# Performance work log

Measured on AMD Instinct MI355X. Metric: run time of the kernel, lower is better.

Reference implementation:

```python
import jax, jax.numpy as jnp
import numpy as np

B, C, L, H, W = 8, 768, 8, 14, 14
HEADS = 12
HD = C // HEADS
SCALE = HD ** (-0.5)
KQ, SQ, PQ = (3, 3, 3), (1, 1, 1), (1, 1, 1)
KKV, SKV, PKV = (3, 3, 3), (1, 2, 2), (1, 1, 1)
EPS = 1e-6


def setup_inputs() -> dict:
    key = jax.random.key(0)
    ks = jax.random.split(key, 16)
    s = 0.02
    inp = {
        'x': jax.random.normal(ks[0], (B, C, L, H, W), jnp.float32),
        'class_token': jax.random.normal(ks[1], (B, C), jnp.float32),
        'Wq': jax.random.normal(ks[2], (C, C), jnp.float32) * s,
        'bq': jnp.zeros((C,), jnp.float32),
        'Wk': jax.random.normal(ks[3], (C, C), jnp.float32) * s,
        'bk': jnp.zeros((C,), jnp.float32),
        'Wv': jax.random.normal(ks[4], (C, C), jnp.float32) * s,
        'bv': jnp.zeros((C,), jnp.float32),
        # depthwise Conv3d kernels: (C, 1, kD, kH, kW), groups=C, no bias
        'conv_q': jax.random.normal(ks[5], (C, 1) + KQ, jnp.float32) * 0.1,
        'conv_k': jax.random.normal(ks[6], (C, 1) + KKV, jnp.float32) * 0.1,
        'conv_v': jax.random.normal(ks[7], (C, 1) + KKV, jnp.float32) * 0.1,
        'lnq_w': jnp.ones((C,), jnp.float32), 'lnq_b': jnp.zeros((C,), jnp.float32),
        'lnk_w': jnp.ones((C,), jnp.float32), 'lnk_b': jnp.zeros((C,), jnp.float32),
        'lnv_w': jnp.ones((C,), jnp.float32), 'lnv_b': jnp.zeros((C,), jnp.float32),
        'Wproj': jax.random.normal(ks[8], (C, C), jnp.float32) * s,
        'bproj': jnp.zeros((C,), jnp.float32),
    }
    return inp


def _linear_keep(x, cls, Wm, b):
    # x: (B,C,l,h,w) -> tokens (B,N,C), prepend cls, linear, split
    Bb, Cc, l, h, w = x.shape
    t = x.reshape(Bb, Cc, -1).transpose(0, 2, 1)          # (B,N,C)
    t = jnp.concatenate([cls[:, None, :], t], axis=1)      # (B,1+N,C)
    y = t @ Wm.T + b
    cls_o = y[:, 0]
    y = y[:, 1:].transpose(0, 2, 1).reshape(Bb, -1, l, h, w)
    return y, cls_o


def _pool(x, wconv, stride, pad, ln_w, ln_b):
    # depthwise 3D conv (groups=C), then LayerNorm over channels
    y = jax.lax.conv_general_dilated(
        x, wconv, window_strides=stride,
        padding=[(p, p) for p in pad],
        dimension_numbers=('NCDHW', 'OIDHW', 'NCDHW'),
        feature_group_count=C)
    y = jnp.moveaxis(y, 1, -1)                            # (B,l,h,w,C)
    mu = y.mean(-1, keepdims=True)
    var = y.var(-1, keepdims=True)
    y = (y - mu) * jax.lax.rsqrt(var + EPS) * ln_w + ln_b
    return jnp.moveaxis(y, -1, 1)


def _to_heads(t):
    # (B,C,l,h,w) -> (B,heads,N,head_dim)
    Bb = t.shape[0]
    return t.reshape(Bb, HEADS, HD, -1).transpose(0, 1, 3, 2)


def _attention(q, k, v, cq, ck, cv, Wp, bp, out_lhw):
    Bb = q.shape[0]
    q = jnp.concatenate([cq.reshape(Bb, HEADS, 1, HD), _to_heads(q)], axis=2)
    k = jnp.concatenate([ck.reshape(Bb, HEADS, 1, HD), _to_heads(k)], axis=2)
    v = jnp.concatenate([cv.reshape(Bb, HEADS, 1, HD), _to_heads(v)], axis=2)
    scores = jnp.einsum('bhqc,bhkc->bhqk', q, k) * SCALE
    attn = jax.nn.softmax(scores, axis=-1)
    o = jnp.einsum('bhqk,bhkc->bhqc', attn, v)            # (B,heads,1+Nq,hd)
    o = o.transpose(0, 2, 1, 3).reshape(Bb, -1, C)        # (B,1+Nq,C)
    o = o @ Wp.T + bp
    cls_o = o[:, 0]
    xo = o[:, 1:].transpose(0, 2, 1).reshape(Bb, C, *out_lhw)
    return xo, cls_o


def reference(x, class_token, Wq, bq, Wk, bk, Wv, bv,
              conv_q, conv_k, conv_v,
              lnq_w, lnq_b, lnk_w, lnk_b, lnv_w, lnv_b,
              Wproj, bproj):
    # pool_first=False: QKV linears first (with cls token), then pooling of the
    # spatial tensors only (cls tokens bypass pooling).
    q, cls_q = _linear_keep(x, class_token, Wq, bq)
    k, cls_k = _linear_keep(x, class_token, Wk, bk)
    v, cls_v = _linear_keep(x, class_token, Wv, bv)
    q = _pool(q, conv_q, SQ, PQ, lnq_w, lnq_b)
    k = _pool(k, conv_k, SKV, PKV, lnk_w, lnk_b)
    v = _pool(v, conv_v, SKV, PKV, lnv_w, lnv_b)
    out_lhw = q.shape[2:]
    return _attention(q, k, v, cls_q, cls_k, cls_v, Wproj, bproj, out_lhw)
```

## Files before the change

### kernel.cpp

```cpp
#include <hip/hip_runtime.h>

#define CDIM 768
#define BATCH 8
#define LDEPTH 8
#define HHEIGHT 14
#define WWIDTH 14
#define NSP 1568
#define NSPX 1576
#define NQTOK 1569
#define NKSP 392
#define NKTOK 393
#define NHEADS 12
#define HEADDIM 64
#define ATTN_SCALE 0.125f
#define LN_EPS 1e-6f
#define MTOK (BATCH * NQTOK)
#define NPAD_X 1792
#define WELEM (CDIM * CDIM)
#define TQP 1792
#define TKP 448

typedef _Float16 f16;
typedef _Float16 f16x8_t __attribute__((ext_vector_type(8)));
typedef _Float16 f16x4_t __attribute__((ext_vector_type(4)));
typedef float f32x4_t __attribute__((ext_vector_type(4)));
typedef float f32x2_t __attribute__((ext_vector_type(2)));

__device__ __forceinline__ void gld_lds16(const void* g, void* l) {
  __builtin_amdgcn_global_load_lds(
      (const __attribute__((address_space(1))) void*)g,
      (__attribute__((address_space(3))) void*)l, 16, 0, 0);
}

__global__ __launch_bounds__(256) void convert4_kernel(
    const float* __restrict__ s0, const float* __restrict__ s1,
    const float* __restrict__ s2, const float* __restrict__ s3,
    f16* __restrict__ dst) {
  const int mat = blockIdx.y;
  const float* src = (mat == 0) ? s0 : (mat == 1) ? s1 : (mat == 2) ? s2 : s3;
  int i = (blockIdx.x * 256 + threadIdx.x) * 4;
  if (i < WELEM) {
    float4 v = *(const float4*)&src[i];
    f16x4_t h = {(f16)v.x, (f16)v.y, (f16)v.z, (f16)v.w};
    *(f16x4_t*)&dst[(size_t)mat * WELEM + i] = h;
  }
}

__global__ __launch_bounds__(256) void transpose_x_kernel(
    const float* __restrict__ X, const float* __restrict__ cls,
    f16* __restrict__ Xt) {
  __shared__ float t[32][33];
  const int b = blockIdx.z;
  const int k0 = blockIdx.y * 32;
  const int n0 = blockIdx.x * 32;
  const int tx = threadIdx.x & 31, ty = threadIdx.x >> 5;
#pragma unroll
  for (int i = 0; i < 4; i++) {
    int k = k0 + ty + i * 8;
    int n = n0 + tx;
    float v;
    if (n < NSP)
      v = X[((size_t)b * CDIM + k) * NSP + n];
    else if (n == NSP)
      v = cls[b * CDIM + k];
    else
      v = 0.f;
    t[ty + i * 8][tx] = v;
  }
  __syncthreads();
#pragma unroll
  for (int i = 0; i < 4; i++) {
    int n = n0 + ty + i * 8;
    Xt[((size_t)b * NPAD_X + n) * CDIM + k0 + tx] = (f16)t[tx][ty + i * 8];
  }
}

__global__ __launch_bounds__(256, 2) void gemm_qkv_f16_kernel(
    const f16* __restrict__ W16, const f16* __restrict__ Xt,
    const float* __restrict__ bq, const float* __restrict__ bk,
    const float* __restrict__ bv, f16* __restrict__ OutBase) {
  __shared__ __align__(16) f16 Asm[128 * 32];
  __shared__ __align__(16) f16 Bsm[256 * 32];

  const int bid = blockIdx.x;
  const int b = bid & 7;
  const int rem = bid >> 3;
  const int mat = rem / 42;
  const int rem2 = rem % 42;
  const int m0 = (rem2 / 7) * 128;
  const int n0 = (rem2 % 7) * 256;
  const int tid = threadIdx.x;
  const int lane = tid & 63;
  const int w = tid >> 6;
  const int wr = w >> 1, wc = w & 1;
  const int l15 = lane & 15, l4 = lane >> 4;

  const f16* A16 = W16 + (size_t)mat * WELEM;
  const float* bias = (mat == 0) ? bq : (mat == 1) ? bk : bv;
  f16* Out = OutBase + (size_t)mat * ((size_t)BATCH * CDIM * NSPX);

  const int srow = lane >> 2;
  const int skq = ((lane & 3) ^ ((lane >> 3) & 3)) * 8;
  const f16* Ag = A16 + (size_t)(m0 + w * 32 + srow) * CDIM + skq;
  const f16* Bg = Xt + ((size_t)b * NPAD_X + n0 + w * 64 + srow) * CDIM + skq;
  f16* lA = Asm + w * 32 * 32;
  f16* lB = Bsm + w * 64 * 32;

  const int rsw = (l15 >> 1) & 3;
  const int kchunk = (l4 ^ rsw) * 8;

  f32x4_t acc[4][8];
#pragma unroll
  for (int i = 0; i < 4; i++)
#pragma unroll
    for (int j = 0; j < 8; j++) acc[i][j] = (f32x4_t){0.f, 0.f, 0.f, 0.f};

  for (int k0 = 0; k0 < CDIM; k0 += 32) {
    gld_lds16(Ag + k0, lA);
    gld_lds16(Ag + 16 * CDIM + k0, lA + 16 * 32);
    gld_lds16(Bg + k0, lB);
    gld_lds16(Bg + 16 * CDIM + k0, lB + 16 * 32);
    gld_lds16(Bg + 32 * CDIM + k0, lB + 32 * 32);
    gld_lds16(Bg + 48 * CDIM + k0, lB + 48 * 32);
    __syncthreads();
    f16x8_t af[4];
#pragma unroll
    for (int mi = 0; mi < 4; mi++)
      af[mi] = *(const f16x8_t*)(Asm + (wr * 64 + mi * 16 + l15) * 32 + kchunk);
#pragma unroll
    for (int ni = 0; ni < 8; ni++) {
      f16x8_t bfv =
          *(const f16x8_t*)(Bsm + (wc * 128 + ni * 16 + l15) * 32 + kchunk);
#pragma unroll
      for (int mi = 0; mi < 4; mi++)
        acc[mi][ni] = __builtin_amdgcn_mfma_f32_16x16x32_f16(
            af[mi], bfv, acc[mi][ni], 0, 0, 0);
    }
    __syncthreads();
  }

#pragma unroll
  for (int mi = 0; mi < 4; mi++) {
    const int mbase = m0 + wr * 64 + mi * 16 + l4 * 4;
#pragma unroll
    for (int ni = 0; ni < 8; ni++) {
      const int n = n0 + wc * 128 + ni * 16 + l15;
      if (n < NQTOK) {
#pragma unroll
        for (int r = 0; r < 4; r++) {
          Out[((size_t)b * CDIM + mbase + r) * NSPX + n] =
              (f16)(acc[mi][ni][r] + bias[mbase + r]);
        }
      }
    }
  }
}

__global__ __launch_bounds__(256, 2) void gemm_proj_f16_kernel(
    const f16* __restrict__ Wp16, const f16* __restrict__ o16,
    const float* __restrict__ bias, float* __restrict__ xo,
    float* __restrict__ cls_o) {
  __shared__ __align__(16) f16 Asm[128 * 32];
  __shared__ __align__(16) f16 Bsm[256 * 32];

  const int bid = blockIdx.x;
  const int xcd = bid & 7, pos_ = bid >> 3;
  const int base = (xcd < 4) ? xcd * 38 : 152 + (xcd - 4) * 37;
  const int wgid = base + pos_;
  const int m0 = (wgid / 50) * 128;
  const int n0 = (wgid % 50) * 256;
  const int tid = threadIdx.x;
  const int lane = tid & 63;
  const int w = tid >> 6;
  const int wr = w >> 1, wc = w & 1;
  const int l15 = lane & 15, l4 = lane >> 4;

  const int srow = lane >> 2;
  const int skq = ((lane & 3) ^ ((lane >> 3) & 3)) * 8;
  const f16* Ag = Wp16 + (size_t)(m0 + srow) * CDIM + skq;
  const f16* Bg = o16 + (size_t)(n0 + w * 64 + srow) * CDIM + skq;
  f16* lA = Asm + w * 32 * 32;
  f16* lB = Bsm + w * 64 * 32;
  const f16* Agw = Ag + (size_t)(w * 32) * CDIM;

  const int rsw = (l15 >> 1) & 3;
  const int kchunk = (l4 ^ rsw) * 8;

  f32x4_t acc[4][8];
#pragma unroll
  for (int i = 0; i < 4; i++)
#pragma unroll
    for (int j = 0; j < 8; j++) acc[i][j] = (f32x4_t){0.f, 0.f, 0.f, 0.f};

  for (int k0 = 0; k0 < CDIM; k0 += 32) {
    gld_lds16(Agw + k0, lA);
    gld_lds16(Agw + 16 * CDIM + k0, lA + 16 * 32);
    gld_lds16(Bg + k0, lB);
    gld_lds16(Bg + 16 * CDIM + k0, lB + 16 * 32);
    gld_lds16(Bg + 32 * CDIM + k0, lB + 32 * 32);
    gld_lds16(Bg + 48 * CDIM + k0, lB + 48 * 32);
    __syncthreads();
    f16x8_t af[4];
#pragma unroll
    for (int mi = 0; mi < 4; mi++)
      af[mi] = *(const f16x8_t*)(Asm + (wr * 64 + mi * 16 + l15) * 32 + kchunk);
#pragma unroll
    for (int ni = 0; ni < 8; ni++) {
      f16x8_t bfv =
          *(const f16x8_t*)(Bsm + (wc * 128 + ni * 16 + l15) * 32 + kchunk);
#pragma unroll
      for (int mi = 0; mi < 4; mi++)
        acc[mi][ni] = __builtin_amdgcn_mfma_f32_16x16x32_f16(
            af[mi], bfv, acc[mi][ni], 0, 0, 0);
    }
    __syncthreads();
  }

#pragma unroll
  for (int ni = 0; ni < 8; ni++) {
    const int tok = n0 + wc * 128 + ni * 16 + l15;
    if (tok < MTOK) {
      const int bb = tok / NQTOK;
      const int nn = tok % NQTOK;
#pragma unroll
      for (int mi = 0; mi < 4; mi++) {
        const int mbase = m0 + wr * 64 + mi * 16 + l4 * 4;
#pragma unroll
        for (int r = 0; r < 4; r++) {
          float v = acc[mi][ni][r] + bias[mbase + r];
          if (nn == 0)
            cls_o[bb * CDIM + mbase + r] = v;
          else
            xo[((size_t)bb * CDIM + mbase + r) * (size_t)NSP + nn - 1] = v;
        }
      }
    }
  }
}

__global__ __launch_bounds__(256) void dwconv_q_kernel(
    const f16* __restrict__ q_lin, const float* __restrict__ cq,
    f16* __restrict__ q_pool) {
  __shared__ float vol[16 * 196];
  __shared__ float wsm[27];
  const int c = blockIdx.x % CDIM;
  const int b = blockIdx.x / CDIM;
  const f16* xb = q_lin + ((size_t)b * CDIM + c) * (size_t)NSPX;

  for (int i = threadIdx.x; i < 16 * 196; i += 256) vol[i] = 0.f;
  if (threadIdx.x < 27) wsm[threadIdx.x] = cq[c * 27 + threadIdx.x];
  __syncthreads();
  for (int i = threadIdx.x; i < NSP; i += 256) {
    int li = i / 196;
    int r = i - li * 196;
    int hi = r / 14;
    int wi = r - hi * 14;
    vol[(wi + 1) * 196 + (hi + 1) * 12 + (li + 1)] = (float)xb[i];
  }
  __syncthreads();

  if (threadIdx.x < 196) {
    const int ho = threadIdx.x / 14;
    const int wo = threadIdx.x - ho * 14;
    float sums[8];
#pragma unroll
    for (int lo = 0; lo < 8; lo++) sums[lo] = 0.f;
#pragma unroll
    for (int kh = 0; kh < 3; kh++) {
#pragma unroll
      for (int kw = 0; kw < 3; kw++) {
        const float* p = &vol[(wo + kw) * 196 + (ho + kh) * 12];
        float z[10];
        *(f32x4_t*)&z[0] = *(const f32x4_t*)p;
        *(f32x4_t*)&z[4] = *(const f32x4_t*)(p + 4);
        *(f32x2_t*)&z[8] = *(const f32x2_t*)(p + 8);
        const float w0 = wsm[0 + kh * 3 + kw];
        const float w1 = wsm[9 + kh * 3 + kw];
        const float w2 = wsm[18 + kh * 3 + kw];
#pragma unroll
        for (int lo = 0; lo < 8; lo++) {
          sums[lo] = fmaf(z[lo], w0, sums[lo]);
          sums[lo] = fmaf(z[lo + 1], w1, sums[lo]);
          sums[lo] = fmaf(z[lo + 2], w2, sums[lo]);
        }
      }
    }
    f16* ob = q_pool + ((size_t)b * CDIM + c) * (size_t)NSP;
    const int hw = ho * 14 + wo;
#pragma unroll
    for (int lo = 0; lo < 8; lo++) ob[lo * 196 + hw] = (f16)sums[lo];
  }
}

__global__ __launch_bounds__(256) void dwconv_kv_kernel(
    const f16* __restrict__ k_lin, const f16* __restrict__ v_lin,
    const float* __restrict__ ck, const float* __restrict__ cv,
    f16* __restrict__ k_pool, f16* __restrict__ v_pool) {
  __shared__ float vol4[4][16 * 196];
  __shared__ float wsm4[4][27];
  const int which = blockIdx.y;
  const f16* X = which ? v_lin : k_lin;
  const float* wconv = which ? cv : ck;
  f16* Out = which ? v_pool : k_pool;
  const int cg = blockIdx.x % (CDIM / 4);
  const int b = blockIdx.x / (CDIM / 4);
  const int c0 = cg * 4;
  const f16* xb0 = X + ((size_t)b * CDIM + c0) * (size_t)NSPX;

  for (int i = threadIdx.x; i < 4 * 16 * 196; i += 256)
    ((float*)vol4)[i] = 0.f;
  if (threadIdx.x < 108) {
    int ch = threadIdx.x / 27;
    int j = threadIdx.x - ch * 27;
    wsm4[ch][j] = wconv[(c0 + ch) * 27 + j];
  }
  __syncthreads();
  for (int i = threadIdx.x; i < 4 * NSP; i += 256) {
    int ch = i / NSP;
    int j = i - ch * NSP;
    int li = j / 196;
    int r = j - li * 196;
    int hi = r / 14;
    int wi = r - hi * 14;
    vol4[ch][(wi + 1) * 196 + (hi + 1) * 12 + (li + 1)] =
        (float)xb0[(size_t)ch * NSPX + j];
  }
  __syncthreads();

  if (threadIdx.x < 196) {
    const int ch = threadIdx.x / 49;
    const int p2 = threadIdx.x - ch * 49;
    const int ho = p2 / 7;
    const int wo = p2 - ho * 7;
    const float* vol = vol4[ch];
    const float* wsm = wsm4[ch];
    float sums[8];
#pragma unroll
    for (int lo = 0; lo < 8; lo++) sums[lo] = 0.f;
#pragma unroll
    for (int kh = 0; kh < 3; kh++) {
#pragma unroll
      for (int kw = 0; kw < 3; kw++) {
        const float* p = &vol[(wo * 2 + kw) * 196 + (ho * 2 + kh) * 12];
        float z[10];
        *(f32x4_t*)&z[0] = *(const f32x4_t*)p;
        *(f32x4_t*)&z[4] = *(const f32x4_t*)(p + 4);
        *(f32x2_t*)&z[8] = *(const f32x2_t*)(p + 8);
        const float w0 = wsm[0 + kh * 3 + kw];
        const float w1 = wsm[9 + kh * 3 + kw];
        const float w2 = wsm[18 + kh * 3 + kw];
#pragma unroll
        for (int lo = 0; lo < 8; lo++) {
          sums[lo] = fmaf(z[lo], w0, sums[lo]);
          sums[lo] = fmaf(z[lo + 1], w1, sums[lo]);
          sums[lo] = fmaf(z[lo + 2], w2, sums[lo]);
        }
      }
    }
    f16* ob = Out + ((size_t)b * CDIM + c0 + ch) * (size_t)NKSP;
    const int hw = ho * 7 + wo;
#pragma unroll
    for (int lo = 0; lo < 8; lo++) ob[lo * 49 + hw] = (f16)sums[lo];
  }
}

__global__ __launch_bounds__(256) void ln_pack_qk2_kernel(
    const f16* __restrict__ qp, const f16* __restrict__ kp,
    const float* __restrict__ lnq_w, const float* __restrict__ lnq_b,
    const float* __restrict__ lnk_w, const float* __restrict__ lnk_b,
    f16* __restrict__ Qh, f16* __restrict__ Kh) {
  const int bx = blockIdx.x;
  const bool isq = bx < 49;
  const f16* xp = isq ? qp : kp;
  const float* ln_w = isq ? lnq_w : lnk_w;
  const float* ln_b = isq ? lnq_b : lnk_b;
  f16* OutH = isq ? Qh : Kh;
  const int np = isq ? NSP : NKSP;
  const int tp = isq ? TQP : TKP;
  const int b = blockIdx.y;
  const int p0 = (isq ? bx : bx - 49) * 32;
  const int tid = threadIdx.x;
  const int pl = tid & 31;
  const int grp = tid >> 5;
  const int pos = p0 + pl;
  const bool act = pos < np;
  const f16* Xb = xp + (size_t)b * CDIM * (size_t)np;

  __shared__ __align__(16) f16 tile[32][784];
  __shared__ float r1[8][33], r2[8][33];
  __shared__ float smean[32], srstd[32];

  const int swz = (pl & 7) << 3;
  float s1 = 0.f, s2 = 0.f;
  for (int cc = 0; cc < 12; cc++) {
    const int c0 = grp * 96 + cc * 8;
    f16x8_t hv;
#pragma unroll
    for (int i = 0; i < 8; i++) {
      f16 h = act ? Xb[(size_t)(c0 + i) * np + pos] : (f16)0.f;
      hv[i] = h;
      float v = (float)h;
      s1 += v;
      s2 = fmaf(v, v, s2);
    }
    *(f16x8_t*)&tile[pl][c0 ^ swz] = hv;
  }
  r1[grp][pl] = s1;
  r2[grp][pl] = s2;
  __syncthreads();
  if (tid < 32) {
    float t1 = 0.f, t2 = 0.f;
#pragma unroll
    for (int g = 0; g < 8; g++) { t1 += r1[g][tid]; t2 += r2[g][tid]; }
    float mean = t1 * (1.f / 768.f);
    float var = t2 * (1.f / 768.f) - mean * mean;
    smean[tid] = mean;
    srstd[tid] = rsqrtf(var + LN_EPS);
  }
  __syncthreads();

  const int tl = tid >> 3, d8 = (tid & 7) * 8;
  const float mean = smean[tl], rstd = srstd[tl];
  const bool wv = (p0 + tl) < np;
  const int tswz = (tl & 7) << 3;
#pragma unroll
  for (int h = 0; h < NHEADS; h++) {
    const int c = h * 64 + d8;
    f16x8_t raw = *(const f16x8_t*)&tile[tl][c ^ tswz];
    float4 w1 = *(const float4*)&ln_w[c];
    float4 w2 = *(const float4*)&ln_w[c + 4];
    float4 b1 = *(const float4*)&ln_b[c];
    float4 b2 = *(const float4*)&ln_b[c + 4];
    f16x8_t ov;
    ov[0] = (f16)(((float)raw[0] - mean) * rstd * w1.x + b1.x);
    ov[1] = (f16)(((float)raw[1] - mean) * rstd * w1.y + b1.y);
    ov[2] = (f16)(((float)raw[2] - mean) * rstd * w1.z + b1.z);
    ov[3] = (f16)(((float)raw[3] - mean) * rstd * w1.w + b1.w);
    ov[4] = (f16)(((float)raw[4] - mean) * rstd * w2.x + b2.x);
    ov[5] = (f16)(((float)raw[5] - mean) * rstd * w2.y + b2.y);
    ov[6] = (f16)(((float)raw[6] - mean) * rstd * w2.z + b2.z);
    ov[7] = (f16)(((float)raw[7] - mean) * rstd * w2.w + b2.w);
    if (wv)
      *(uint4*)(OutH +
                (((size_t)(b * NHEADS + h)) * (size_t)tp + (p0 + tl + 1)) * 64 +
                d8) = *(uint4*)&ov;
  }
}

__global__ __launch_bounds__(256) void ln_pack_v_kernel(
    const f16* __restrict__ vp, const f16* __restrict__ vlin,
    const float* __restrict__ ln_w, const float* __restrict__ ln_b,
    f16* __restrict__ Vht) {
  const int b = blockIdx.y;
  const int t0 = blockIdx.x * 32;
  const int tid = threadIdx.x;
  const int pl = tid & 31;
  const int grp = tid >> 5;
  const int t = t0 + pl;
  const int pos = t - 1;
  const bool isv = (t >= 1) && (t < NKTOK);
  const f16* Vb = vp + (size_t)b * CDIM * (size_t)NKSP;

  __shared__ float r1[8][33], r2[8][33];
  __shared__ float smean[32], srstd[32];
  __shared__ __align__(16) f16 vtile[128][40];

  float s1 = 0.f, s2 = 0.f;
  if (isv) {
    for (int c = grp; c < CDIM; c += 8) {
      float v = (float)Vb[(size_t)c * NKSP + pos];
      s1 += v;
      s2 = fmaf(v, v, s2);
    }
  }
  r1[grp][pl] = s1;
  r2[grp][pl] = s2;
  __syncthreads();
  if (tid < 32) {
    float t1 = 0.f, t2 = 0.f;
#pragma unroll
    for (int g = 0; g < 8; g++) { t1 += r1[g][tid]; t2 += r2[g][tid]; }
    float mean = t1 * (1.f / 768.f);
    float var = t2 * (1.f / 768.f) - mean * mean;
    smean[tid] = mean;
    srstd[tid] = rsqrtf(var + LN_EPS);
  }
  __syncthreads();
  const float mean = smean[pl], rstd = srstd[pl];

  for (int cc = 0; cc < 6; cc++) {
#pragma unroll
    for (int i = 0; i < 16; i++) {
      int cl = grp * 16 + i;
      int c = cc * 128 + cl;
      float outv;
      if (isv)
        outv = ((float)Vb[(size_t)c * NKSP + pos] - mean) * rstd * ln_w[c] +
               ln_b[c];
      else if (t == 0)
        outv = (float)vlin[((size_t)b * CDIM + c) * NSPX + NSP];
      else
        outv = 0.f;
      vtile[cl][pl] = (f16)outv;
    }
    __syncthreads();
#pragma unroll
    for (int it = 0; it < 2; it++) {
      int idx = it * 256 + tid;
      int cl = idx >> 2, t8 = (idx & 3) * 8;
      uint4 vv = *(const uint4*)&vtile[cl][t8];
      *(uint4*)(Vht + ((size_t)b * CDIM + cc * 128 + cl) * (size_t)TKP + t0 +
                t8) = vv;
    }
    __syncthreads();
  }
}

__global__ __launch_bounds__(768) void cls_fill_kernel(
    const f16* __restrict__ qlin, const f16* __restrict__ klin,
    f16* __restrict__ Qh, f16* __restrict__ Kh) {
  const int b = blockIdx.x;
  const int c = threadIdx.x;
  Qh[(((size_t)(b * NHEADS + (c >> 6))) * TQP) * 64 + (c & 63)] =
      qlin[((size_t)b * CDIM + c) * NSPX + NSP];
  Kh[(((size_t)(b * NHEADS + (c >> 6))) * TKP) * 64 + (c & 63)] =
      klin[((size_t)b * CDIM + c) * NSPX + NSP];
}

__global__ __launch_bounds__(256) void attn_mfma_kernel(
    const f16* __restrict__ Qh, const f16* __restrict__ Kh,
    const f16* __restrict__ Vht, f16* __restrict__ o16) {
  __shared__ __align__(16) f16 Ks[64 * 72];
  __shared__ __align__(16) f16 Vt[64 * 72];
  const int qt = blockIdx.x, h = blockIdx.y, b = blockIdx.z;
  const int tid = threadIdx.x;
  const int lane = tid & 63;
  const int w = tid >> 6;
  const int l15 = lane & 15, l4 = lane >> 4;
  const int q0 = qt * 256 + w * 64;

  const f16* Qp = Qh + ((size_t)(b * NHEADS + h) * TQP) * 64;
  const f16* Kp = Kh + ((size_t)(b * NHEADS + h) * TKP) * 64;
  const f16* Vp = Vht + ((size_t)(b * NHEADS + h) * 64) * TKP;

  f16x8_t bq[4][2];
#pragma unroll
  for (int qi = 0; qi < 4; qi++)
#pragma unroll
    for (int kf = 0; kf < 2; kf++)
      bq[qi][kf] = *(const f16x8_t*)(Qp + (size_t)(q0 + qi * 16 + l15) * 64 +
                                     kf * 32 + l4 * 8);

  f32x4_t oacc[4][4];
#pragma unroll
  for (int df = 0; df < 4; df++)
#pragma unroll
    for (int qi = 0; qi < 4; qi++) oacc[df][qi] = (f32x4_t){0.f, 0.f, 0.f, 0.f};
  float mrow[4] = {-1e30f, -1e30f, -1e30f, -1e30f};
  float lrow[4] = {0.f, 0.f, 0.f, 0.f};

  const int sr = tid >> 2, sc = (tid & 3) * 16;

  for (int kv0 = 0; kv0 < TKP; kv0 += 64) {
    const f16* kg = Kp + (size_t)(kv0 + sr) * 64 + sc;
    uint4 kl0 = *(const uint4*)kg;
    uint4 kl1 = *(const uint4*)(kg + 8);
    const f16* vg = Vp + (size_t)sr * TKP + kv0 + sc;
    uint4 vl0 = *(const uint4*)vg;
    uint4 vl1 = *(const uint4*)(vg + 8);
    __syncthreads();
    *(uint4*)(Ks + sr * 72 + sc) = kl0;
    *(uint4*)(Ks + sr * 72 + sc + 8) = kl1;
    *(uint4*)(Vt + sr * 72 + sc) = vl0;
    *(uint4*)(Vt + sr * 72 + sc + 8) = vl1;
    __syncthreads();

    f32x4_t sacc[4][4];
#pragma unroll
    for (int ki = 0; ki < 4; ki++)
#pragma unroll
      for (int qi = 0; qi < 4; qi++)
        sacc[ki][qi] = (f32x4_t){0.f, 0.f, 0.f, 0.f};
#pragma unroll
    for (int kf = 0; kf < 2; kf++) {
#pragma unroll
      for (int ki = 0; ki < 4; ki++) {
        f16x8_t ak =
            *(const f16x8_t*)(Ks + (ki * 16 + l15) * 72 + kf * 32 + l4 * 8);
#pragma unroll
        for (int qi = 0; qi < 4; qi++)
          sacc[ki][qi] = __builtin_amdgcn_mfma_f32_16x16x32_f16(
              ak, bq[qi][kf], sacc[ki][qi], 0, 0, 0);
      }
    }

    float pmax[4] = {-1e30f, -1e30f, -1e30f, -1e30f};
#pragma unroll
    for (int ki = 0; ki < 4; ki++) {
      const int keyb = kv0 + ki * 16 + l4 * 4;
#pragma unroll
      for (int qi = 0; qi < 4; qi++) {
#pragma unroll
        for (int rr = 0; rr < 4; rr++) {
          float s = sacc[ki][qi][rr] * ATTN_SCALE;
          if (keyb + rr >= NKTOK) s = -1e30f;
          sacc[ki][qi][rr] = s;
          pmax[qi] = fmaxf(pmax[qi], s);
        }
      }
    }
#pragma unroll
    for (int qi = 0; qi < 4; qi++) {
      pmax[qi] = fmaxf(pmax[qi], __shfl_xor(pmax[qi], 16, 64));
      pmax[qi] = fmaxf(pmax[qi], __shfl_xor(pmax[qi], 32, 64));
      float mnew = fmaxf(mrow[qi], pmax[qi]);
      float alpha = __expf(mrow[qi] - mnew);
      mrow[qi] = mnew;
      lrow[qi] *= alpha;
#pragma unroll
      for (int df = 0; df < 4; df++) {
        oacc[df][qi][0] *= alpha;
        oacc[df][qi][1] *= alpha;
        oacc[df][qi][2] *= alpha;
        oacc[df][qi][3] *= alpha;
      }
    }

#pragma unroll
    for (int ki = 0; ki < 4; ki++) {
      f16x4_t pb[4];
#pragma unroll
      for (int qi = 0; qi < 4; qi++) {
        float p0 = __expf(sacc[ki][qi][0] - mrow[qi]);
        float p1 = __expf(sacc[ki][qi][1] - mrow[qi]);
        float p2 = __expf(sacc[ki][qi][2] - mrow[qi]);
        float p3 = __expf(sacc[ki][qi][3] - mrow[qi]);
        lrow[qi] += p0 + p1 + p2 + p3;
        f16x4_t pv = {(f16)p0, (f16)p1, (f16)p2, (f16)p3};
        pb[qi] = pv;
      }
#pragma unroll
      for (int df = 0; df < 4; df++) {
        f16x4_t av =
            *(const f16x4_t*)(Vt + (df * 16 + l15) * 72 + ki * 16 + l4 * 4);
#pragma unroll
        for (int qi = 0; qi < 4; qi++)
          oacc[df][qi] = __builtin_amdgcn_mfma_f32_16x16x16f16(
              av, pb[qi], oacc[df][qi], 0, 0, 0);
      }
    }
  }

  float inv[4];
#pragma unroll
  for (int qi = 0; qi < 4; qi++) {
    float l = lrow[qi];
    l += __shfl_xor(l, 16, 64);
    l += __shfl_xor(l, 32, 64);
    inv[qi] = 1.f / l;
  }
#pragma unroll
  for (int qi = 0; qi < 4; qi++) {
    const int q = q0 + qi * 16 + l15;
    if (q < NQTOK) {
      f16* op = o16 + ((size_t)(b * NQTOK + q)) * CDIM + h * 64 + l4 * 4;
#pragma unroll
      for (int df = 0; df < 4; df++) {
        f16x4_t ov = {(f16)(oacc[df][qi][0] * inv[qi]),
                      (f16)(oacc[df][qi][1] * inv[qi]),
                      (f16)(oacc[df][qi][2] * inv[qi]),
                      (f16)(oacc[df][qi][3] * inv[qi])};
        *(f16x4_t*)(op + df * 16) = ov;
      }
    }
  }
}

extern "C" void kernel_launch(void* const* d_in, const int* in_sizes, int n_in,
                              void* d_out, int out_size, void* d_ws, size_t ws_size,
                              hipStream_t stream) {
  const float* x      = (const float*)d_in[0];
  const float* cls    = (const float*)d_in[1];
  const float* Wq     = (const float*)d_in[2];
  const float* bq     = (const float*)d_in[3];
  const float* Wk     = (const float*)d_in[4];
  const float* bk     = (const float*)d_in[5];
  const float* Wv     = (const float*)d_in[6];
  const float* bv     = (const float*)d_in[7];
  const float* conv_q = (const float*)d_in[8];
  const float* conv_k = (const float*)d_in[9];
  const float* conv_v = (const float*)d_in[10];
  const float* lnq_w  = (const float*)d_in[11];
  const float* lnq_b  = (const float*)d_in[12];
  const float* lnk_w  = (const float*)d_in[13];
  const float* lnk_b  = (const float*)d_in[14];
  const float* lnv_w  = (const float*)d_in[15];
  const float* lnv_b  = (const float*)d_in[16];
  const float* Wproj  = (const float*)d_in[17];
  const float* bproj  = (const float*)d_in[18];

  char* wsb = (char*)d_ws;
  f16*   Xt     = (f16*)(wsb + 0);
  f16*   W16    = (f16*)(wsb + 22020096);
  f16*   q_lin  = (f16*)(wsb + 26738688);
  f16*   k_lin  = (f16*)(wsb + 46104576);
  f16*   v_lin  = (f16*)(wsb + 65470464);
  f16*   k_pool = (f16*)(wsb + 84836352);
  f16*   v_pool = (f16*)(wsb + 89653248);
  f16*   Kh     = (f16*)(wsb + 94470144);
  f16*   Vht    = (f16*)(wsb + 99975168);
  f16*   q_pool = (f16*)(wsb + 105480192);
  f16*   Qh     = Xt;
  f16*   o16    = v_lin;

  f16* W16p = W16 + (size_t)3 * WELEM;

  convert4_kernel<<<dim3(576, 4), 256, 0, stream>>>(Wq, Wk, Wv, Wproj, W16);

  transpose_x_kernel<<<dim3(56, 24, BATCH), 256, 0, stream>>>(x, cls, Xt);

  gemm_qkv_f16_kernel<<<1008, 256, 0, stream>>>(W16, Xt, bq, bk, bv, q_lin);

  cls_fill_kernel<<<BATCH, 768, 0, stream>>>(q_lin, k_lin, Qh, Kh);

  dwconv_q_kernel<<<BATCH * CDIM, 256, 0, stream>>>(q_lin, conv_q, q_pool);
  dwconv_kv_kernel<<<dim3(BATCH * CDIM / 4, 2), 256, 0, stream>>>(
      k_lin, v_lin, conv_k, conv_v, k_pool, v_pool);

  ln_pack_qk2_kernel<<<dim3(62, BATCH), 256, 0, stream>>>(
      q_pool, k_pool, lnq_w, lnq_b, lnk_w, lnk_b, Qh, Kh);
  ln_pack_v_kernel<<<dim3(14, BATCH), 256, 0, stream>>>(v_pool, v_lin, lnv_w,
                                                        lnv_b, Vht);

  attn_mfma_kernel<<<dim3(7, NHEADS, BATCH), 256, 0, stream>>>(Qh, Kh, Vht,
                                                               o16);

  float* xo = (float*)d_out;
  float* cls_o = (float*)d_out + (size_t)BATCH * CDIM * NSP;
  gemm_proj_f16_kernel<<<300, 256, 0, stream>>>(W16p, o16, bproj, xo, cls_o);
}
```

Measured before the change: 329.7 us.

## Load weight fragments directly from global into registers with prefetch in GEMMs

Result: slower. 357.0 us (+8.3%).

```diff
diff --git a/kernel.cpp b/kernel.cpp
--- a/kernel.cpp
+++ b/kernel.cpp
@@ -79,7 +79,6 @@
     const f16* __restrict__ W16, const f16* __restrict__ Xt,
     const float* __restrict__ bq, const float* __restrict__ bk,
     const float* __restrict__ bv, f16* __restrict__ OutBase) {
-  __shared__ __align__(16) f16 Asm[128 * 32];
   __shared__ __align__(16) f16 Bsm[256 * 32];
 
   const int bid = blockIdx.x;
@@ -101,32 +100,38 @@
 
   const int srow = lane >> 2;
   const int skq = ((lane & 3) ^ ((lane >> 3) & 3)) * 8;
-  const f16* Ag = A16 + (size_t)(m0 + w * 32 + srow) * CDIM + skq;
   const f16* Bg = Xt + ((size_t)b * NPAD_X + n0 + w * 64 + srow) * CDIM + skq;
-  f16* lA = Asm + w * 32 * 32;
   f16* lB = Bsm + w * 64 * 32;
 
   const int rsw = (l15 >> 1) & 3;
   const int kchunk = (l4 ^ rsw) * 8;
 
+  const f16* Afrag = A16 + (size_t)(m0 + wr * 64 + l15) * CDIM + l4 * 8;
+
   f32x4_t acc[4][8];
 #pragma unroll
   for (int i = 0; i < 4; i++)
 #pragma unroll
     for (int j = 0; j < 8; j++) acc[i][j] = (f32x4_t){0.f, 0.f, 0.f, 0.f};
 
-  for (int k0 = 0; k0 < CDIM; k0 += 32) {
-    gld_lds16(Ag + k0, lA);
-    gld_lds16(Ag + 16 * CDIM + k0, lA + 16 * 32);
+  f16x8_t afc[4], afn[4];
+#pragma unroll
+  for (int mi = 0; mi < 4; mi++)
+    afc[mi] = *(const f16x8_t*)(Afrag + (size_t)(mi * 16) * CDIM);
+
+  for (int t = 0; t < CDIM / 32; ++t) {
+    const int k0 = t * 32;
     gld_lds16(Bg + k0, lB);
     gld_lds16(Bg + 16 * CDIM + k0, lB + 16 * 32);
     gld_lds16(Bg + 32 * CDIM + k0, lB + 32 * 32);
     gld_lds16(Bg + 48 * CDIM + k0, lB + 48 * 32);
+    if (t + 1 < CDIM / 32) {
+#pragma unroll
+      for (int mi = 0; mi < 4; mi++)
+        afn[mi] =
+            *(const f16x8_t*)(Afrag + (size_t)(mi * 16) * CDIM + k0 + 32);
+    }
     __syncthreads();
-    f16x8_t af[4];
-#pragma unroll
-    for (int mi = 0; mi < 4; mi++)
-      af[mi] = *(const f16x8_t*)(Asm + (wr * 64 + mi * 16 + l15) * 32 + kchunk);
 #pragma unroll
     for (int ni = 0; ni < 8; ni++) {
       f16x8_t bfv =
@@ -134,9 +139,11 @@
 #pragma unroll
       for (int mi = 0; mi < 4; mi++)
         acc[mi][ni] = __builtin_amdgcn_mfma_f32_16x16x32_f16(
-            af[mi], bfv, acc[mi][ni], 0, 0, 0);
+            afc[mi], bfv, acc[mi][ni], 0, 0, 0);
     }
     __syncthreads();
+#pragma unroll
+    for (int mi = 0; mi < 4; mi++) afc[mi] = afn[mi];
   }
 
 #pragma unroll
@@ -160,7 +167,6 @@
     const f16* __restrict__ Wp16, const f16* __restrict__ o16,
     const float* __restrict__ bias, float* __restrict__ xo,
     float* __restrict__ cls_o) {
-  __shared__ __align__(16) f16 Asm[128 * 32];
   __shared__ __align__(16) f16 Bsm[256 * 32];
 
   const int bid = blockIdx.x;
@@ -177,33 +183,38 @@
 
   const int srow = lane >> 2;
   const int skq = ((lane & 3) ^ ((lane >> 3) & 3)) * 8;
-  const f16* Ag = Wp16 + (size_t)(m0 + srow) * CDIM + skq;
   const f16* Bg = o16 + (size_t)(n0 + w * 64 + srow) * CDIM + skq;
-  f16* lA = Asm + w * 32 * 32;
   f16* lB = Bsm + w * 64 * 32;
-  const f16* Agw = Ag + (size_t)(w * 32) * CDIM;
 
   const int rsw = (l15 >> 1) & 3;
   const int kchunk = (l4 ^ rsw) * 8;
 
+  const f16* Afrag = Wp16 + (size_t)(m0 + wr * 64 + l15) * CDIM + l4 * 8;
+
   f32x4_t acc[4][8];
 #pragma unroll
   for (int i = 0; i < 4; i++)
 #pragma unroll
     for (int j = 0; j < 8; j++) acc[i][j] = (f32x4_t){0.f, 0.f, 0.f, 0.f};
 
-  for (int k0 = 0; k0 < CDIM; k0 += 32) {
-    gld_lds16(Agw + k0, lA);
-    gld_lds16(Agw + 16 * CDIM + k0, lA + 16 * 32);
+  f16x8_t afc[4], afn[4];
+#pragma unroll
+  for (int mi = 0; mi < 4; mi++)
+    afc[mi] = *(const f16x8_t*)(Afrag + (size_t)(mi * 16) * CDIM);
+
+  for (int t = 0; t < CDIM / 32; ++t) {
+    const int k0 = t * 32;
     gld_lds16(Bg + k0, lB);
     gld_lds16(Bg + 16 * CDIM + k0, lB + 16 * 32);
     gld_lds16(Bg + 32 * CDIM + k0, lB + 32 * 32);
     gld_lds16(Bg + 48 * CDIM + k0, lB + 48 * 32);
+    if (t + 1 < CDIM / 32) {
+#pragma unroll
+      for (int mi = 0; mi < 4; mi++)
+        afn[mi] =
+            *(const f16x8_t*)(Afrag + (size_t)(mi * 16) * CDIM + k0 + 32);
+    }
     __syncthreads();
-    f16x8_t af[4];
-#pragma unroll
-    for (int mi = 0; mi < 4; mi++)
-      af[mi] = *(const f16x8_t*)(Asm + (wr * 64 + mi * 16 + l15) * 32 + kchunk);
 #pragma unroll
     for (int ni = 0; ni < 8; ni++) {
       f16x8_t bfv =
@@ -211,9 +222,11 @@
 #pragma unroll
       for (int mi = 0; mi < 4; mi++)
         acc[mi][ni] = __builtin_amdgcn_mfma_f32_16x16x32_f16(
-            af[mi], bfv, acc[mi][ni], 0, 0, 0);
+            afc[mi], bfv, acc[mi][ni], 0, 0, 0);
     }
     __syncthreads();
+#pragma unroll
+    for (int mi = 0; mi < 4; mi++) afc[mi] = afn[mi];
   }
 
 #pragma unroll
```

## Double-buffer LDS in QKV and projection GEMMs, fold cls fill into LN pack

Applied to the files above, without the earlier changes.

Measured after the change: 331.1 us. About the same (+0.4%).

```diff
diff --git a/kernel.cpp b/kernel.cpp
--- a/kernel.cpp
+++ b/kernel.cpp
@@ -79,8 +79,8 @@
     const f16* __restrict__ W16, const f16* __restrict__ Xt,
     const float* __restrict__ bq, const float* __restrict__ bk,
     const float* __restrict__ bv, f16* __restrict__ OutBase) {
-  __shared__ __align__(16) f16 Asm[128 * 32];
-  __shared__ __align__(16) f16 Bsm[256 * 32];
+  __shared__ __align__(16) f16 Asm[2][128 * 32];
+  __shared__ __align__(16) f16 Bsm[2][256 * 32];
 
   const int bid = blockIdx.x;
   const int b = bid & 7;
@@ -103,8 +103,8 @@
   const int skq = ((lane & 3) ^ ((lane >> 3) & 3)) * 8;
   const f16* Ag = A16 + (size_t)(m0 + w * 32 + srow) * CDIM + skq;
   const f16* Bg = Xt + ((size_t)b * NPAD_X + n0 + w * 64 + srow) * CDIM + skq;
-  f16* lA = Asm + w * 32 * 32;
-  f16* lB = Bsm + w * 64 * 32;
+  const int lAofs = w * 32 * 32;
+  const int lBofs = w * 64 * 32;
 
   const int rsw = (l15 >> 1) & 3;
   const int kchunk = (l4 ^ rsw) * 8;
@@ -115,28 +115,42 @@
 #pragma unroll
     for (int j = 0; j < 8; j++) acc[i][j] = (f32x4_t){0.f, 0.f, 0.f, 0.f};
 
-  for (int k0 = 0; k0 < CDIM; k0 += 32) {
-    gld_lds16(Ag + k0, lA);
-    gld_lds16(Ag + 16 * CDIM + k0, lA + 16 * 32);
-    gld_lds16(Bg + k0, lB);
-    gld_lds16(Bg + 16 * CDIM + k0, lB + 16 * 32);
-    gld_lds16(Bg + 32 * CDIM + k0, lB + 32 * 32);
-    gld_lds16(Bg + 48 * CDIM + k0, lB + 48 * 32);
-    __syncthreads();
+  gld_lds16(Ag, Asm[0] + lAofs);
+  gld_lds16(Ag + 16 * CDIM, Asm[0] + lAofs + 16 * 32);
+  gld_lds16(Bg, Bsm[0] + lBofs);
+  gld_lds16(Bg + 16 * CDIM, Bsm[0] + lBofs + 16 * 32);
+  gld_lds16(Bg + 32 * CDIM, Bsm[0] + lBofs + 32 * 32);
+  gld_lds16(Bg + 48 * CDIM, Bsm[0] + lBofs + 48 * 32);
+  __syncthreads();
+
+  int cur = 0;
+  for (int t = 0; t < CDIM / 32; ++t) {
+    if (t + 1 < CDIM / 32) {
+      const int k1 = (t + 1) * 32;
+      gld_lds16(Ag + k1, Asm[cur ^ 1] + lAofs);
+      gld_lds16(Ag + 16 * CDIM + k1, Asm[cur ^ 1] + lAofs + 16 * 32);
+      gld_lds16(Bg + k1, Bsm[cur ^ 1] + lBofs);
+      gld_lds16(Bg + 16 * CDIM + k1, Bsm[cur ^ 1] + lBofs + 16 * 32);
+      gld_lds16(Bg + 32 * CDIM + k1, Bsm[cur ^ 1] + lBofs + 32 * 32);
+      gld_lds16(Bg + 48 * CDIM + k1, Bsm[cur ^ 1] + lBofs + 48 * 32);
+    }
+    const f16* As = Asm[cur];
+    const f16* Bs = Bsm[cur];
     f16x8_t af[4];
 #pragma unroll
     for (int mi = 0; mi < 4; mi++)
-      af[mi] = *(const f16x8_t*)(Asm + (wr * 64 + mi * 16 + l15) * 32 + kchunk);
+      af[mi] = *(const f16x8_t*)(As + (wr * 64 + mi * 16 + l15) * 32 + kchunk);
 #pragma unroll
     for (int ni = 0; ni < 8; ni++) {
       f16x8_t bfv =
-          *(const f16x8_t*)(Bsm + (wc * 128 + ni * 16 + l15) * 32 + kchunk);
+          *(const f16x8_t*)(Bs + (wc * 128 + ni * 16 + l15) * 32 + kchunk);
 #pragma unroll
       for (int mi = 0; mi < 4; mi++)
         acc[mi][ni] = __builtin_amdgcn_mfma_f32_16x16x32_f16(
             af[mi], bfv, acc[mi][ni], 0, 0, 0);
     }
     __syncthreads();
+    cur ^= 1;
   }
 
 #pragma unroll
@@ -160,8 +174,8 @@
     const f16* __restrict__ Wp16, const f16* __restrict__ o16,
     const float* __restrict__ bias, float* __restrict__ xo,
     float* __restrict__ cls_o) {
-  __shared__ __align__(16) f16 Asm[128 * 32];
-  __shared__ __align__(16) f16 Bsm[256 * 32];
+  __shared__ __align__(16) f16 Asm[2][128 * 32];
+  __shared__ __align__(16) f16 Bsm[2][256 * 32];
 
   const int bid = blockIdx.x;
   const int xcd = bid & 7, pos_ = bid >> 3;
@@ -177,11 +191,10 @@
 
   const int srow = lane >> 2;
   const int skq = ((lane & 3) ^ ((lane >> 3) & 3)) * 8;
-  const f16* Ag = Wp16 + (size_t)(m0 + srow) * CDIM + skq;
+  const f16* Ag = Wp16 + (size_t)(m0 + w * 32 + srow) * CDIM + skq;
   const f16* Bg = o16 + (size_t)(n0 + w * 64 + srow) * CDIM + skq;
-  f16* lA = Asm + w * 32 * 32;
-  f16* lB = Bsm + w * 64 * 32;
-  const f16* Agw = Ag + (size_t)(w * 32) * CDIM;
+  const int lAofs = w * 32 * 32;
+  const int lBofs = w * 64 * 32;
 
   const int rsw = (l15 >> 1) & 3;
   const int kchunk = (l4 ^ rsw) * 8;
@@ -192,28 +205,42 @@
 #pragma unroll
     for (int j = 0; j < 8; j++) acc[i][j] = (f32x4_t){0.f, 0.f, 0.f, 0.f};
 
-  for (int k0 = 0; k0 < CDIM; k0 += 32) {
-    gld_lds16(Agw + k0, lA);
-    gld_lds16(Agw + 16 * CDIM + k0, lA + 16 * 32);
-    gld_lds16(Bg + k0, lB);
-    gld_lds16(Bg + 16 * CDIM + k0, lB + 16 * 32);
-    gld_lds16(Bg + 32 * CDIM + k0, lB + 32 * 32);
-    gld_lds16(Bg + 48 * CDIM + k0, lB + 48 * 32);
-    __syncthreads();
+  gld_lds16(Ag, Asm[0] + lAofs);
+  gld_lds16(Ag + 16 * CDIM, Asm[0] + lAofs + 16 * 32);
+  gld_lds16(Bg, Bsm[0] + lBofs);
+  gld_lds16(Bg + 16 * CDIM, Bsm[0] + lBofs + 16 * 32);
+  gld_lds16(Bg + 32 * CDIM, Bsm[0] + lBofs + 32 * 32);
+  gld_lds16(Bg + 48 * CDIM, Bsm[0] + lBofs + 48 * 32);
+  __syncthreads();
+
+  int cur = 0;
+  for (int t = 0; t < CDIM / 32; ++t) {
+    if (t + 1 < CDIM / 32) {
+      const int k1 = (t + 1) * 32;
+      gld_lds16(Ag + k1, Asm[cur ^ 1] + lAofs);
+      gld_lds16(Ag + 16 * CDIM + k1, Asm[cur ^ 1] + lAofs + 16 * 32);
+      gld_lds16(Bg + k1, Bsm[cur ^ 1] + lBofs);
+      gld_lds16(Bg + 16 * CDIM + k1, Bsm[cur ^ 1] + lBofs + 16 * 32);
+      gld_lds16(Bg + 32 * CDIM + k1, Bsm[cur ^ 1] + lBofs + 32 * 32);
+      gld_lds16(Bg + 48 * CDIM + k1, Bsm[cur ^ 1] + lBofs + 48 * 32);
+    }
+    const f16* As = Asm[cur];
+    const f16* Bs = Bsm[cur];
     f16x8_t af[4];
 #pragma unroll
     for (int mi = 0; mi < 4; mi++)
-      af[mi] = *(const f16x8_t*)(Asm + (wr * 64 + mi * 16 + l15) * 32 + kchunk);
+      af[mi] = *(const f16x8_t*)(As + (wr * 64 + mi * 16 + l15) * 32 + kchunk);
 #pragma unroll
     for (int ni = 0; ni < 8; ni++) {
       f16x8_t bfv =
-          *(const f16x8_t*)(Bsm + (wc * 128 + ni * 16 + l15) * 32 + kchunk);
+          *(const f16x8_t*)(Bs + (wc * 128 + ni * 16 + l15) * 32 + kchunk);
 #pragma unroll
       for (int mi = 0; mi < 4; mi++)
         acc[mi][ni] = __builtin_amdgcn_mfma_f32_16x16x32_f16(
             af[mi], bfv, acc[mi][ni], 0, 0, 0);
     }
     __syncthreads();
+    cur ^= 1;
   }
 
 #pragma unroll
@@ -366,10 +393,26 @@
 
 __global__ __launch_bounds__(256) void ln_pack_qk2_kernel(
     const f16* __restrict__ qp, const f16* __restrict__ kp,
+    const f16* __restrict__ qlin, const f16* __restrict__ klin,
     const float* __restrict__ lnq_w, const float* __restrict__ lnq_b,
     const float* __restrict__ lnk_w, const float* __restrict__ lnk_b,
     f16* __restrict__ Qh, f16* __restrict__ Kh) {
   const int bx = blockIdx.x;
+  const int b = blockIdx.y;
+  const int tid = threadIdx.x;
+
+  if (bx == 62) {
+#pragma unroll
+    for (int cc = 0; cc < 3; cc++) {
+      const int c = tid + cc * 256;
+      Qh[(((size_t)(b * NHEADS + (c >> 6))) * TQP) * 64 + (c & 63)] =
+          qlin[((size_t)b * CDIM + c) * NSPX + NSP];
+      Kh[(((size_t)(b * NHEADS + (c >> 6))) * TKP) * 64 + (c & 63)] =
+          klin[((size_t)b * CDIM + c) * NSPX + NSP];
+    }
+    return;
+  }
+
   const bool isq = bx < 49;
   const f16* xp = isq ? qp : kp;
   const float* ln_w = isq ? lnq_w : lnk_w;
@@ -377,9 +420,7 @@
   f16* OutH = isq ? Qh : Kh;
   const int np = isq ? NSP : NKSP;
   const int tp = isq ? TQP : TKP;
-  const int b = blockIdx.y;
   const int p0 = (isq ? bx : bx - 49) * 32;
-  const int tid = threadIdx.x;
   const int pl = tid & 31;
   const int grp = tid >> 5;
   const int pos = p0 + pl;
@@ -514,17 +555,6 @@
     }
     __syncthreads();
   }
-}
-
-__global__ __launch_bounds__(768) void cls_fill_kernel(
-    const f16* __restrict__ qlin, const f16* __restrict__ klin,
-    f16* __restrict__ Qh, f16* __restrict__ Kh) {
-  const int b = blockIdx.x;
-  const int c = threadIdx.x;
-  Qh[(((size_t)(b * NHEADS + (c >> 6))) * TQP) * 64 + (c & 63)] =
-      qlin[((size_t)b * CDIM + c) * NSPX + NSP];
-  Kh[(((size_t)(b * NHEADS + (c >> 6))) * TKP) * 64 + (c & 63)] =
-      klin[((size_t)b * CDIM + c) * NSPX + NSP];
 }
 
 __global__ __launch_bounds__(256) void attn_mfma_kernel(
@@ -721,14 +751,12 @@
 
   gemm_qkv_f16_kernel<<<1008, 256, 0, stream>>>(W16, Xt, bq, bk, bv, q_lin);
 
-  cls_fill_kernel<<<BATCH, 768, 0, stream>>>(q_lin, k_lin, Qh, Kh);
-
   dwconv_q_kernel<<<BATCH * CDIM, 256, 0, stream>>>(q_lin, conv_q, q_pool);
   dwconv_kv_kernel<<<dim3(BATCH * CDIM / 4, 2), 256, 0, stream>>>(
       k_lin, v_lin, conv_k, conv_v, k_pool, v_pool);
 
-  ln_pack_qk2_kernel<<<dim3(62, BATCH), 256, 0, stream>>>(
-      q_pool, k_pool, lnq_w, lnq_b, lnk_w, lnk_b, Qh, Kh);
+  ln_pack_qk2_kernel<<<dim3(63, BATCH), 256, 0, stream>>>(
+      q_pool, k_pool, q_lin, k_lin, lnq_w, lnq_b, lnk_w, lnk_b, Qh, Kh);
   ln_pack_v_kernel<<<dim3(14, BATCH), 256, 0, stream>>>(v_pool, v_lin, lnv_w,
                                                         lnv_b, Vht);
 
```
